# Optimization experiments

Measured on AMD Instinct MI355X. Metric: run time of the kernel, lower is better.

## Reference

```python
import jax, jax.numpy as jnp
import numpy as np

TEMP = 11.313708498984761  # sqrt(d_k=128)

def setup_inputs() -> dict:
    key = jax.random.key(0)
    ks = jax.random.split(key, 5)
    B, H, T, D = 8, 8, 1024, 128
    shp = (B, H, T, D)
    return {
        "q_time": jax.random.normal(ks[0], shp, dtype=jnp.float32),
        "k_time": jax.random.normal(ks[1], shp, dtype=jnp.float32),
        "q_feature": jax.random.normal(ks[2], shp, dtype=jnp.float32),
        "k_feature": jax.random.normal(ks[3], shp, dtype=jnp.float32),
        "v": jax.random.normal(ks[4], shp, dtype=jnp.float32),
    }

def reference(q_time, k_time, q_feature, k_feature, v):
    # time attention: [B,H,T,T]
    scores_t = jnp.einsum("bhtd,bhsd->bhts", q_time / TEMP, k_time)
    attn_time = jax.nn.softmax(scores_t, axis=-1)
    # feature attention: q_feature^T @ k_feature -> [B,H,D,D]
    scores_f = jnp.einsum("bhtd,bhte->bhde", q_feature / TEMP, k_feature)
    attn_feature = jax.nn.softmax(scores_f, axis=-1)
    # output = attn_time @ v @ attn_feature : [B,H,T,D]
    tv = jnp.einsum("bhts,bhsd->bhtd", attn_time, v)
    output = jnp.einsum("bhtd,bhde->bhte", tv, attn_feature)
    return output, attn_time, attn_feature
```

## Files before the change

kernel.cpp:

```cpp
#include <hip/hip_runtime.h>

typedef __bf16 bf16x8 __attribute__((ext_vector_type(8)));
typedef __bf16 bf16x4 __attribute__((ext_vector_type(4)));
typedef float f32x4 __attribute__((ext_vector_type(4)));

#define T_DIM 1024
#define D_DIM 128
#define NHEAD 64

static constexpr float INV_TEMP = 0.08838834764831845f;
static constexpr size_t OUT_ATTN = (size_t)NHEAD * T_DIM * D_DIM;
static constexpr size_t OUT_AF = OUT_ATTN + (size_t)NHEAD * T_DIM * T_DIM;

#define MFMA16 __builtin_amdgcn_mfma_f32_16x16x32_bf16

__device__ __forceinline__ int swz(int row, int col) {
  return (row << 7) + ((((col >> 3) ^ row) & 15) << 3) + (col & 7);
}

__device__ __forceinline__ bf16x8 ld8(const __bf16* buf, int row, int col) {
  return *reinterpret_cast<const bf16x8*>(&buf[swz(row, col)]);
}

__device__ __forceinline__ void nt_store4(float* dst, float a, float b, float c, float d) {
  f32x4 v = {a, b, c, d};
  __builtin_nontemporal_store(v, reinterpret_cast<f32x4*>(dst));
}

__device__ __forceinline__ void stage_f32_tile_128(const float* __restrict__ src,
                                                   __bf16* dst, int tid, float scale) {
  const float4* s4 = reinterpret_cast<const float4*>(src);
#pragma unroll
  for (int i = 0; i < 16; ++i) {
    int flat = i * 256 + tid;
    int row = flat >> 5;
    int c4 = (flat & 31) << 2;
    float4 vq = s4[flat];
    bf16x4 b;
    b[0] = (__bf16)(vq.x * scale);
    b[1] = (__bf16)(vq.y * scale);
    b[2] = (__bf16)(vq.z * scale);
    b[3] = (__bf16)(vq.w * scale);
    *reinterpret_cast<bf16x4*>(&dst[swz(row, c4)]) = b;
  }
}

__device__ __forceinline__ void stage_wt_tile(const __bf16* __restrict__ src,
                                              __bf16* dst, int tid) {
#pragma unroll
  for (int i = 0; i < 8; ++i) {
    int flat = i * 256 + tid;
    int row = flat >> 4;
    int c8 = (flat & 15) << 3;
    bf16x8 vv = *reinterpret_cast<const bf16x8*>(src + (size_t)row * T_DIM + c8);
    *reinterpret_cast<bf16x8*>(&dst[swz(row, c8)]) = vv;
  }
}

__device__ __forceinline__ void cp16_async(const void* g, void* l) {
  typedef __attribute__((address_space(1))) unsigned int gu32;
  typedef __attribute__((address_space(3))) unsigned int lu32;
  __builtin_amdgcn_global_load_lds((gu32*)g, (lu32*)l, 16, 0, 0);
}

__device__ __forceinline__ void stage_async_tile(const __bf16* __restrict__ gbase,
                                                 int row_stride_elems,
                                                 __bf16* lbuf, int tid) {
  const int w = tid >> 6;
  const int lane = tid & 63;
#pragma unroll
  for (int i = 0; i < 8; ++i) {
    int seg = i * 4 + w;
    int row = seg * 4 + (lane >> 4);
    int c = ((lane & 15) ^ row) & 15;
    const void* src = (const void*)(gbase + (size_t)row * row_stride_elems + c * 8);
    void* dst = (void*)(lbuf + seg * 512);
    cp16_async(src, dst);
  }
}

__device__ __forceinline__ void compute_S(const bf16x8 afrag[4][2], const __bf16* bufB,
                                          int l16, int quad, f32x4 sacc[2][8]) {
#pragma unroll
  for (int mt = 0; mt < 2; ++mt)
#pragma unroll
    for (int nt = 0; nt < 8; ++nt)
      sacc[mt][nt] = (f32x4){0.f, 0.f, 0.f, 0.f};
#pragma unroll
  for (int ki = 0; ki < 4; ++ki) {
    bf16x8 bfr[8];
#pragma unroll
    for (int nt = 0; nt < 8; ++nt)
      bfr[nt] = ld8(bufB, nt * 16 + l16, ki * 32 + quad * 8);
#pragma unroll
    for (int nt = 0; nt < 8; ++nt) {
      sacc[0][nt] = MFMA16(afrag[ki][0], bfr[nt], sacc[0][nt], 0, 0, 0);
      sacc[1][nt] = MFMA16(afrag[ki][1], bfr[nt], sacc[1][nt], 0, 0, 0);
    }
  }
}

__global__ __launch_bounds__(256, 2)
void cd_attn_feature(const float* __restrict__ qf, const float* __restrict__ kf,
                     float* __restrict__ out) {
  __shared__ __bf16 qfT[64][40];
  __shared__ __bf16 kfT[128][40];
  const int tid = threadIdx.x;
  const int w = tid >> 6;
  const int lane = tid & 63;
  const int quad = lane >> 4;
  const int l16 = lane & 15;
  const int head = blockIdx.x & 63;
  const int dstart = (blockIdx.x >> 6) << 6;

  const float* __restrict__ qfh = qf + (size_t)head * (T_DIM * D_DIM);
  const float* __restrict__ kfh = kf + (size_t)head * (T_DIM * D_DIM);

  f32x4 acc[8];
#pragma unroll
  for (int nt = 0; nt < 8; ++nt) acc[nt] = (f32x4){0.f, 0.f, 0.f, 0.f};

  for (int tc = 0; tc < T_DIM; tc += 32) {
    __syncthreads();
#pragma unroll
    for (int i = 0; i < 2; ++i) {
      int flat = i * 256 + tid;
      int t = flat >> 4;
      int d4 = (flat & 15) << 2;
      float4 vv = *reinterpret_cast<const float4*>(qfh + (size_t)(tc + t) * D_DIM + dstart + d4);
      qfT[d4 + 0][t] = (__bf16)vv.x;
      qfT[d4 + 1][t] = (__bf16)vv.y;
      qfT[d4 + 2][t] = (__bf16)vv.z;
      qfT[d4 + 3][t] = (__bf16)vv.w;
    }
#pragma unroll
    for (int i = 0; i < 4; ++i) {
      int flat = i * 256 + tid;
      int t = flat >> 5;
      int e4 = (flat & 31) << 2;
      float4 vv = *reinterpret_cast<const float4*>(kfh + (size_t)(tc + t) * D_DIM + e4);
      kfT[e4 + 0][t] = (__bf16)vv.x;
      kfT[e4 + 1][t] = (__bf16)vv.y;
      kfT[e4 + 2][t] = (__bf16)vv.z;
      kfT[e4 + 3][t] = (__bf16)vv.w;
    }
    __syncthreads();
    bf16x8 a = *reinterpret_cast<const bf16x8*>(&qfT[w * 16 + l16][quad * 8]);
#pragma unroll
    for (int nt = 0; nt < 8; ++nt) {
      bf16x8 b = *reinterpret_cast<const bf16x8*>(&kfT[nt * 16 + l16][quad * 8]);
      acc[nt] = MFMA16(a, b, acc[nt], 0, 0, 0);
    }
  }

  float p[8][4];
  float rsum[4] = {0.f, 0.f, 0.f, 0.f};
#pragma unroll
  for (int nt = 0; nt < 8; ++nt)
#pragma unroll
    for (int r = 0; r < 4; ++r) {
      p[nt][r] = __expf(acc[nt][r] * INV_TEMP);
      rsum[r] += p[nt][r];
    }
#pragma unroll
  for (int off = 1; off < 16; off <<= 1)
#pragma unroll
    for (int r = 0; r < 4; ++r)
      rsum[r] += __shfl_xor(rsum[r], off, 64);
#pragma unroll
  for (int r = 0; r < 4; ++r) rsum[r] = 1.0f / rsum[r];

  float* __restrict__ afh = out + OUT_AF + (size_t)head * (D_DIM * D_DIM);
#pragma unroll
  for (int nt = 0; nt < 8; ++nt)
#pragma unroll
    for (int r = 0; r < 4; ++r)
      afh[(size_t)(dstart + w * 16 + quad * 4 + r) * D_DIM + nt * 16 + l16] = p[nt][r] * rsum[r];
}

__global__ __launch_bounds__(256, 2)
void cd_attn_w(const float* __restrict__ v, const float* __restrict__ out_ro,
               __bf16* __restrict__ wt,
               const float* __restrict__ qt, const float* __restrict__ kt,
               __bf16* __restrict__ qtb, __bf16* __restrict__ ktb) {
  __shared__ __bf16 vt[128 * 128];
  __shared__ __bf16 aft[128 * 128];
  const int tid = threadIdx.x;
  const int w = tid >> 6;
  const int lane = tid & 63;
  const int quad = lane >> 4;
  const int l16 = lane & 15;
  const int head = blockIdx.x & 63;
  const int t0 = (blockIdx.x >> 6) << 7;

  if (qtb != nullptr) {
    const float4* q4 = reinterpret_cast<const float4*>(qt);
    const float4* k4 = reinterpret_cast<const float4*>(kt);
    size_t base = (size_t)blockIdx.x * 2048 + tid;
#pragma unroll
    for (int i = 0; i < 8; ++i) {
      size_t c = base + (size_t)(i * 256);
      float4 a = q4[c * 2], b = q4[c * 2 + 1];
      bf16x8 o;
      o[0] = (__bf16)(a.x * INV_TEMP); o[1] = (__bf16)(a.y * INV_TEMP);
      o[2] = (__bf16)(a.z * INV_TEMP); o[3] = (__bf16)(a.w * INV_TEMP);
      o[4] = (__bf16)(b.x * INV_TEMP); o[5] = (__bf16)(b.y * INV_TEMP);
      o[6] = (__bf16)(b.z * INV_TEMP); o[7] = (__bf16)(b.w * INV_TEMP);
      *reinterpret_cast<bf16x8*>(qtb + c * 8) = o;
      a = k4[c * 2]; b = k4[c * 2 + 1];
      o[0] = (__bf16)a.x; o[1] = (__bf16)a.y; o[2] = (__bf16)a.z; o[3] = (__bf16)a.w;
      o[4] = (__bf16)b.x; o[5] = (__bf16)b.y; o[6] = (__bf16)b.z; o[7] = (__bf16)b.w;
      *reinterpret_cast<bf16x8*>(ktb + c * 8) = o;
    }
  }

  const float* __restrict__ vh = v + (size_t)head * (T_DIM * D_DIM);
  const float* __restrict__ afh = out_ro + OUT_AF + (size_t)head * (D_DIM * D_DIM);

#pragma unroll
  for (int i = 0; i < 16; ++i) {
    int flat = i * 256 + tid;
    int d = flat >> 5;
    int e4 = (flat & 31) << 2;
    float4 vv = *reinterpret_cast<const float4*>(afh + (size_t)d * D_DIM + e4);
    aft[swz(e4 + 0, d)] = (__bf16)vv.x;
    aft[swz(e4 + 1, d)] = (__bf16)vv.y;
    aft[swz(e4 + 2, d)] = (__bf16)vv.z;
    aft[swz(e4 + 3, d)] = (__bf16)vv.w;
  }
  stage_f32_tile_128(vh + (size_t)t0 * D_DIM, vt, tid, 1.0f);
  __syncthreads();

  f32x4 acc[2][8];
#pragma unroll
  for (int mt = 0; mt < 2; ++mt)
#pragma unroll
    for (int nt = 0; nt < 8; ++nt) acc[mt][nt] = (f32x4){0.f, 0.f, 0.f, 0.f};

#pragma unroll
  for (int ki = 0; ki < 4; ++ki) {
    bf16x8 a0 = ld8(vt, w * 32 + l16, ki * 32 + quad * 8);
    bf16x8 a1 = ld8(vt, w * 32 + 16 + l16, ki * 32 + quad * 8);
#pragma unroll
    for (int nt = 0; nt < 8; ++nt) {
      bf16x8 b = ld8(aft, nt * 16 + l16, ki * 32 + quad * 8);
      acc[0][nt] = MFMA16(a0, b, acc[0][nt], 0, 0, 0);
      acc[1][nt] = MFMA16(a1, b, acc[1][nt], 0, 0, 0);
    }
  }

  __syncthreads();
#pragma unroll
  for (int mt = 0; mt < 2; ++mt)
#pragma unroll
    for (int nt = 0; nt < 8; ++nt)
#pragma unroll
      for (int r = 0; r < 4; ++r)
        aft[swz(nt * 16 + l16, w * 32 + mt * 16 + quad * 4 + r)] = (__bf16)acc[mt][nt][r];
  __syncthreads();

  __bf16* __restrict__ wth = wt + (size_t)head * (D_DIM * T_DIM);
#pragma unroll
  for (int i = 0; i < 8; ++i) {
    int row = i * 16 + (tid >> 4);
    int pc = tid & 15;
    bf16x8 vv = *reinterpret_cast<const bf16x8*>(&aft[(row << 7) + (pc << 3)]);
    int col = ((pc ^ row) & 15) << 3;
    *reinterpret_cast<bf16x8*>(&wth[(size_t)row * T_DIM + t0 + col]) = vv;
  }
}

__global__ __launch_bounds__(256, 2)
void cd_attn_time_v2(const __bf16* __restrict__ qtb, const __bf16* __restrict__ ktb,
                     const __bf16* __restrict__ wt, float* __restrict__ out) {
  __shared__ __align__(16) __bf16 lds_all[2 * 128 * 128];
  __bf16* buf0 = lds_all;
  __bf16* buf1 = lds_all + 128 * 128;
  const int tid = threadIdx.x;
  const int w = tid >> 6;
  const int lane = tid & 63;
  const int quad = lane >> 4;
  const int l16 = lane & 15;
  const int head = blockIdx.x & 63;
  const int t0 = (blockIdx.x >> 6) << 7;

  const __bf16* __restrict__ qth = qtb + (size_t)head * (T_DIM * D_DIM);
  const __bf16* __restrict__ kth = ktb + (size_t)head * (T_DIM * D_DIM);
  const __bf16* __restrict__ wth = wt + (size_t)head * (D_DIM * T_DIM);
  float* __restrict__ attn_out = out + OUT_ATTN + (size_t)head * ((size_t)T_DIM * T_DIM);
  float* __restrict__ o_out = out + (size_t)head * (T_DIM * D_DIM);

  stage_async_tile(kth, D_DIM, buf0, tid);
  bf16x8 afrag[4][2];
#pragma unroll
  for (int ki = 0; ki < 4; ++ki) {
#pragma unroll
    for (int mt = 0; mt < 2; ++mt)
      afrag[ki][mt] = *reinterpret_cast<const bf16x8*>(
          qth + (size_t)(t0 + w * 32 + mt * 16 + l16) * D_DIM + ki * 32 + quad * 8);
  }

  float rs[2][4] = {{0.f, 0.f, 0.f, 0.f}, {0.f, 0.f, 0.f, 0.f}};
  for (int j = 0; j < 8; ++j) {
    if (j < 7) {
      stage_async_tile(kth + (size_t)(j + 1) * (128 * D_DIM), D_DIM,
                       (j & 1) ? buf0 : buf1, tid);
      asm volatile("s_waitcnt vmcnt(8)" ::: "memory");
    } else {
      asm volatile("s_waitcnt vmcnt(0)" ::: "memory");
    }
    __builtin_amdgcn_s_barrier();
    f32x4 sacc[2][8];
    compute_S(afrag, (j & 1) ? buf1 : buf0, l16, quad, sacc);
#pragma unroll
    for (int mt = 0; mt < 2; ++mt)
#pragma unroll
      for (int nt = 0; nt < 8; ++nt)
#pragma unroll
        for (int r = 0; r < 4; ++r)
          rs[mt][r] += __expf(sacc[mt][nt][r]);
    asm volatile("s_waitcnt lgkmcnt(0)" ::: "memory");
    __builtin_amdgcn_s_barrier();
  }
#pragma unroll
  for (int off = 1; off < 16; off <<= 1)
#pragma unroll
    for (int mt = 0; mt < 2; ++mt)
#pragma unroll
      for (int r = 0; r < 4; ++r)
        rs[mt][r] += __shfl_xor(rs[mt][r], off, 64);
  float invl[2][4];
#pragma unroll
  for (int mt = 0; mt < 2; ++mt)
#pragma unroll
    for (int r = 0; r < 4; ++r)
      invl[mt][r] = 1.0f / rs[mt][r];

  f32x4 uacc[2][8];
#pragma unroll
  for (int mt = 0; mt < 2; ++mt)
#pragma unroll
    for (int nt = 0; nt < 8; ++nt) uacc[mt][nt] = (f32x4){0.f, 0.f, 0.f, 0.f};

  stage_async_tile(kth, D_DIM, buf0, tid);
  stage_async_tile(wth, T_DIM, buf1, tid);
  for (int j = 0; j < 8; ++j) {
    if (j == 0)
      asm volatile("s_waitcnt vmcnt(0)" ::: "memory");
    else
      asm volatile("s_waitcnt vmcnt(16)" ::: "memory");
    __builtin_amdgcn_s_barrier();
    f32x4 sacc[2][8];
    compute_S(afrag, buf0, l16, quad, sacc);
    asm volatile("s_waitcnt lgkmcnt(0)" ::: "memory");
    __builtin_amdgcn_s_barrier();
#pragma unroll
    for (int mt = 0; mt < 2; ++mt)
#pragma unroll
      for (int nt = 0; nt < 8; ++nt)
#pragma unroll
        for (int r = 0; r < 4; ++r)
          buf0[swz(w * 32 + mt * 16 + quad * 4 + r, nt * 16 + l16)] =
              (__bf16)(__expf(sacc[mt][nt][r]) * invl[mt][r]);
    asm volatile("s_waitcnt lgkmcnt(0)" ::: "memory");
#pragma unroll
    for (int ki = 0; ki < 4; ++ki) {
      bf16x8 aP0 = ld8(buf0, w * 32 + l16, ki * 32 + quad * 8);
      bf16x8 aP1 = ld8(buf0, w * 32 + 16 + l16, ki * 32 + quad * 8);
#pragma unroll
      for (int nt = 0; nt < 8; ++nt) {
        bf16x8 bW = ld8(buf1, nt * 16 + l16, ki * 32 + quad * 8);
        uacc[0][nt] = MFMA16(aP0, bW, uacc[0][nt], 0, 0, 0);
        uacc[1][nt] = MFMA16(aP1, bW, uacc[1][nt], 0, 0, 0);
      }
    }
    asm volatile("s_waitcnt lgkmcnt(0)" ::: "memory");
    __builtin_amdgcn_s_barrier();
    bf16x8 pv[8];
#pragma unroll
    for (int i = 0; i < 8; ++i) {
      int row = i * 16 + (tid >> 4);
      int pc = tid & 15;
      pv[i] = *reinterpret_cast<const bf16x8*>(&buf0[(row << 7) + (pc << 3)]);
    }
    asm volatile("s_waitcnt lgkmcnt(0)" ::: "memory");
    __builtin_amdgcn_s_barrier();
    if (j < 7) {
      stage_async_tile(kth + (size_t)(j + 1) * (128 * D_DIM), D_DIM, buf0, tid);
      stage_async_tile(wth + (size_t)(j + 1) * 128, T_DIM, buf1, tid);
    }
    asm volatile("" ::: "memory");
    __builtin_amdgcn_sched_barrier(0);
    const int s0 = j * 128;
#pragma unroll
    for (int i = 0; i < 8; ++i) {
      int row = i * 16 + (tid >> 4);
      int pc = tid & 15;
      int col = ((pc ^ row) & 15) << 3;
      float* dst = attn_out + (size_t)(t0 + row) * T_DIM + s0 + col;
      nt_store4(dst, (float)pv[i][0], (float)pv[i][1], (float)pv[i][2], (float)pv[i][3]);
      nt_store4(dst + 4, (float)pv[i][4], (float)pv[i][5], (float)pv[i][6], (float)pv[i][7]);
    }
  }

  float* fbuf = reinterpret_cast<float*>(lds_all);
#pragma unroll
  for (int mt = 0; mt < 2; ++mt)
#pragma unroll
    for (int nt = 0; nt < 8; ++nt)
#pragma unroll
      for (int r = 0; r < 4; ++r)
        fbuf[(w * 32 + mt * 16 + quad * 4 + r) * 128 + nt * 16 + l16] = uacc[mt][nt][r];
  asm volatile("s_waitcnt lgkmcnt(0)" ::: "memory");
  __builtin_amdgcn_s_barrier();
#pragma unroll
  for (int i = 0; i < 16; ++i) {
    int flat = i * 256 + tid;
    int row = flat >> 5;
    int c4 = (flat & 31) << 2;
    f32x4 vv = *reinterpret_cast<const f32x4*>(&fbuf[row * 128 + c4]);
    __builtin_nontemporal_store(
        vv, reinterpret_cast<f32x4*>(o_out + (size_t)(t0 + row) * D_DIM + c4));
  }
}

__global__ __launch_bounds__(256, 2)
void cd_attn_time(const float* __restrict__ qt, const float* __restrict__ kt,
                  const __bf16* __restrict__ wt, float* __restrict__ out) {
  __shared__ __bf16 bufB[128 * 128];
  __shared__ __bf16 bufP[128 * 128];
  const int tid = threadIdx.x;
  const int w = tid >> 6;
  const int lane = tid & 63;
  const int quad = lane >> 4;
  const int l16 = lane & 15;
  const int head = blockIdx.x & 63;
  const int t0 = (blockIdx.x >> 6) << 7;

  const float* __restrict__ qth = qt + (size_t)head * (T_DIM * D_DIM);
  const float* __restrict__ kth = kt + (size_t)head * (T_DIM * D_DIM);
  const __bf16* __restrict__ wth = wt + (size_t)head * (D_DIM * T_DIM);
  float* __restrict__ attn_out = out + OUT_ATTN + (size_t)head * ((size_t)T_DIM * T_DIM);
  float* __restrict__ o_out = out + (size_t)head * (T_DIM * D_DIM);

  stage_f32_tile_128(qth + (size_t)t0 * D_DIM, bufB, tid, INV_TEMP);
  __syncthreads();
  bf16x8 afrag[4][2];
#pragma unroll
  for (int ki = 0; ki < 4; ++ki) {
    afrag[ki][0] = ld8(bufB, w * 32 + l16, ki * 32 + quad * 8);
    afrag[ki][1] = ld8(bufB, w * 32 + 16 + l16, ki * 32 + quad * 8);
  }

  float rs[2][4] = {{0.f, 0.f, 0.f, 0.f}, {0.f, 0.f, 0.f, 0.f}};
  for (int j = 0; j < 8; ++j) {
    __syncthreads();
    stage_f32_tile_128(kth + (size_t)(j * 128) * D_DIM, bufB, tid, 1.0f);
    __syncthreads();
    f32x4 sacc[2][8];
    compute_S(afrag, bufB, l16, quad, sacc);
#pragma unroll
    for (int mt = 0; mt < 2; ++mt)
#pragma unroll
      for (int nt = 0; nt < 8; ++nt)
#pragma unroll
        for (int r = 0; r < 4; ++r)
          rs[mt][r] += __expf(sacc[mt][nt][r]);
  }
#pragma unroll
  for (int off = 1; off < 16; off <<= 1)
#pragma unroll
    for (int mt = 0; mt < 2; ++mt)
#pragma unroll
      for (int r = 0; r < 4; ++r)
        rs[mt][r] += __shfl_xor(rs[mt][r], off, 64);
  float invl[2][4];
#pragma unroll
  for (int mt = 0; mt < 2; ++mt)
#pragma unroll
    for (int r = 0; r < 4; ++r)
      invl[mt][r] = 1.0f / rs[mt][r];

  f32x4 uacc[2][8];
#pragma unroll
  for (int mt = 0; mt < 2; ++mt)
#pragma unroll
    for (int nt = 0; nt < 8; ++nt) uacc[mt][nt] = (f32x4){0.f, 0.f, 0.f, 0.f};

  for (int j = 0; j < 8; ++j) {
    __syncthreads();
    stage_f32_tile_128(kth + (size_t)(j * 128) * D_DIM, bufB, tid, 1.0f);
    __syncthreads();
    f32x4 sacc[2][8];
    compute_S(afrag, bufB, l16, quad, sacc);
    __syncthreads();
    stage_wt_tile(wth + j * 128, bufB, tid);
#pragma unroll
    for (int mt = 0; mt < 2; ++mt)
#pragma unroll
      for (int nt = 0; nt < 8; ++nt)
#pragma unroll
        for (int r = 0; r < 4; ++r) {
          float p = __expf(sacc[mt][nt][r]) * invl[mt][r];
          bufP[swz(w * 32 + mt * 16 + quad * 4 + r, nt * 16 + l16)] = (__bf16)p;
        }
    __syncthreads();
    const int s0 = j * 128;
#pragma unroll
    for (int i = 0; i < 8; ++i) {
      int row = i * 16 + (tid >> 4);
      int pc = tid & 15;
      bf16x8 pv = *reinterpret_cast<const bf16x8*>(&bufP[(row << 7) + (pc << 3)]);
      int col = ((pc ^ row) & 15) << 3;
      float4 o1, o2;
      o1.x = (float)pv[0]; o1.y = (float)pv[1]; o1.z = (float)pv[2]; o1.w = (float)pv[3];
      o2.x = (float)pv[4]; o2.y = (float)pv[5]; o2.z = (float)pv[6]; o2.w = (float)pv[7];
      float4* dstp = reinterpret_cast<float4*>(attn_out + (size_t)(t0 + row) * T_DIM + s0 + col);
      dstp[0] = o1;
      dstp[1] = o2;
    }
#pragma unroll
    for (int ki = 0; ki < 4; ++ki) {
      bf16x8 aP0 = ld8(bufP, w * 32 + l16, ki * 32 + quad * 8);
      bf16x8 aP1 = ld8(bufP, w * 32 + 16 + l16, ki * 32 + quad * 8);
#pragma unroll
      for (int nt = 0; nt < 8; ++nt) {
        bf16x8 bW = ld8(bufB, nt * 16 + l16, ki * 32 + quad * 8);
        uacc[0][nt] = MFMA16(aP0, bW, uacc[0][nt], 0, 0, 0);
        uacc[1][nt] = MFMA16(aP1, bW, uacc[1][nt], 0, 0, 0);
      }
    }
  }

#pragma unroll
  for (int mt = 0; mt < 2; ++mt)
#pragma unroll
    for (int nt = 0; nt < 8; ++nt)
#pragma unroll
      for (int r = 0; r < 4; ++r)
        o_out[(size_t)(t0 + w * 32 + mt * 16 + quad * 4 + r) * D_DIM + nt * 16 + l16] =
            uacc[mt][nt][r];
}

extern "C" void kernel_launch(void* const* d_in, const int* in_sizes, int n_in,
                              void* d_out, int out_size, void* d_ws, size_t ws_size,
                              hipStream_t stream) {
  (void)in_sizes; (void)n_in; (void)out_size;
  const float* q_time    = (const float*)d_in[0];
  const float* k_time    = (const float*)d_in[1];
  const float* q_feature = (const float*)d_in[2];
  const float* k_feature = (const float*)d_in[3];
  const float* v         = (const float*)d_in[4];
  float* out = (float*)d_out;
  __bf16* wt = (__bf16*)d_ws;

  const size_t NELEM = (size_t)NHEAD * T_DIM * D_DIM;
  const size_t WS_NEED = NELEM * 2 * 3;

  if (ws_size >= WS_NEED) {
    __bf16* qtb = wt + NELEM;
    __bf16* ktb = qtb + NELEM;
    cd_attn_feature<<<128, 256, 0, stream>>>(q_feature, k_feature, out);
    cd_attn_w<<<512, 256, 0, stream>>>(v, out, wt, q_time, k_time, qtb, ktb);
    cd_attn_time_v2<<<512, 256, 0, stream>>>(qtb, ktb, wt, out);
  } else {
    cd_attn_w<<<512, 256, 0, stream>>>(v, out, wt, nullptr, nullptr, nullptr, nullptr);
    cd_attn_time<<<512, 256, 0, stream>>>(q_time, k_time, wt, out);
  }
}
```

Measured before the change: 680.0 us.

## Double query rows per block to share K and W tiles across eight waves

The time-attention kernel now uses 512-thread blocks covering 256 query rows, so each staged K and W tile in LDS serves twice as many rows and fewer blocks reload the same data. The first pass moves from a double buffer to a triple buffer for K, prefetching two tiles ahead and issuing the next load after the barrier. P is written into a split slab (S2 for the first four waves, S0 for the rest), and the output epilogue is done in two halves. LDS use rises to 96KB per block, and only 256 blocks are launched, which may lower occupancy and latency hiding. The fallback path also gains a feature-attention launch.

Result: slower. 712.6 us (+4.8%).

```diff
diff --git a/kernel.cpp b/kernel.cpp
--- a/kernel.cpp
+++ b/kernel.cpp
@@ -63,14 +63,14 @@
   __builtin_amdgcn_global_load_lds((gu32*)g, (lu32*)l, 16, 0, 0);
 }
 
-__device__ __forceinline__ void stage_async_tile(const __bf16* __restrict__ gbase,
-                                                 int row_stride_elems,
-                                                 __bf16* lbuf, int tid) {
+__device__ __forceinline__ void stage_async_tile512(const __bf16* __restrict__ gbase,
+                                                    int row_stride_elems,
+                                                    __bf16* lbuf, int tid) {
   const int w = tid >> 6;
   const int lane = tid & 63;
 #pragma unroll
-  for (int i = 0; i < 8; ++i) {
-    int seg = i * 4 + w;
+  for (int i = 0; i < 4; ++i) {
+    int seg = i * 8 + w;
     int row = seg * 4 + (lane >> 4);
     int c = ((lane & 15) ^ row) & 15;
     const void* src = (const void*)(gbase + (size_t)row * row_stride_elems + c * 8);
@@ -270,19 +270,20 @@
   }
 }
 
-__global__ __launch_bounds__(256, 2)
-void cd_attn_time_v2(const __bf16* __restrict__ qtb, const __bf16* __restrict__ ktb,
+__global__ __launch_bounds__(512, 2)
+void cd_attn_time_v3(const __bf16* __restrict__ qtb, const __bf16* __restrict__ ktb,
                      const __bf16* __restrict__ wt, float* __restrict__ out) {
-  __shared__ __align__(16) __bf16 lds_all[2 * 128 * 128];
-  __bf16* buf0 = lds_all;
-  __bf16* buf1 = lds_all + 128 * 128;
+  __shared__ __align__(16) __bf16 lds_all[3 * 16384];
+  __bf16* S0 = lds_all;
+  __bf16* S1 = lds_all + 16384;
+  __bf16* S2 = lds_all + 32768;
   const int tid = threadIdx.x;
   const int w = tid >> 6;
   const int lane = tid & 63;
   const int quad = lane >> 4;
   const int l16 = lane & 15;
   const int head = blockIdx.x & 63;
-  const int t0 = (blockIdx.x >> 6) << 7;
+  const int t0 = (blockIdx.x >> 6) << 8;
 
   const __bf16* __restrict__ qth = qtb + (size_t)head * (T_DIM * D_DIM);
   const __bf16* __restrict__ kth = ktb + (size_t)head * (T_DIM * D_DIM);
@@ -290,7 +291,8 @@
   float* __restrict__ attn_out = out + OUT_ATTN + (size_t)head * ((size_t)T_DIM * T_DIM);
   float* __restrict__ o_out = out + (size_t)head * (T_DIM * D_DIM);
 
-  stage_async_tile(kth, D_DIM, buf0, tid);
+  stage_async_tile512(kth, D_DIM, S0, tid);
+  stage_async_tile512(kth + (size_t)128 * D_DIM, D_DIM, S1, tid);
   bf16x8 afrag[4][2];
 #pragma unroll
   for (int ki = 0; ki < 4; ++ki) {
@@ -302,16 +304,16 @@
 
   float rs[2][4] = {{0.f, 0.f, 0.f, 0.f}, {0.f, 0.f, 0.f, 0.f}};
   for (int j = 0; j < 8; ++j) {
-    if (j < 7) {
-      stage_async_tile(kth + (size_t)(j + 1) * (128 * D_DIM), D_DIM,
-                       (j & 1) ? buf0 : buf1, tid);
-      asm volatile("s_waitcnt vmcnt(8)" ::: "memory");
-    } else {
+    if (j < 7)
+      asm volatile("s_waitcnt vmcnt(4)" ::: "memory");
+    else
       asm volatile("s_waitcnt vmcnt(0)" ::: "memory");
-    }
-    __builtin_amdgcn_s_barrier();
+    __builtin_amdgcn_s_barrier();
+    if (j < 6)
+      stage_async_tile512(kth + (size_t)(j + 2) * (128 * D_DIM), D_DIM,
+                          lds_all + ((j + 2) % 3) * 16384, tid);
     f32x4 sacc[2][8];
-    compute_S(afrag, (j & 1) ? buf1 : buf0, l16, quad, sacc);
+    compute_S(afrag, lds_all + (j % 3) * 16384, l16, quad, sacc);
 #pragma unroll
     for (int mt = 0; mt < 2; ++mt)
 #pragma unroll
@@ -342,8 +344,11 @@
 #pragma unroll
     for (int nt = 0; nt < 8; ++nt) uacc[mt][nt] = (f32x4){0.f, 0.f, 0.f, 0.f};
 
-  stage_async_tile(kth, D_DIM, buf0, tid);
-  stage_async_tile(wth, T_DIM, buf1, tid);
+  __bf16* pslab = (w < 4) ? S2 : S0;
+  const int prow0 = (w & 3) * 32;
+
+  stage_async_tile512(kth, D_DIM, S0, tid);
+  stage_async_tile512(wth, T_DIM, S1, tid);
   for (int j = 0; j < 8; ++j) {
     if (j == 0)
       asm volatile("s_waitcnt vmcnt(0)" ::: "memory");
@@ -351,7 +356,7 @@
       asm volatile("s_waitcnt vmcnt(16)" ::: "memory");
     __builtin_amdgcn_s_barrier();
     f32x4 sacc[2][8];
-    compute_S(afrag, buf0, l16, quad, sacc);
+    compute_S(afrag, S0, l16, quad, sacc);
     asm volatile("s_waitcnt lgkmcnt(0)" ::: "memory");
     __builtin_amdgcn_s_barrier();
 #pragma unroll
@@ -360,16 +365,16 @@
       for (int nt = 0; nt < 8; ++nt)
 #pragma unroll
         for (int r = 0; r < 4; ++r)
-          buf0[swz(w * 32 + mt * 16 + quad * 4 + r, nt * 16 + l16)] =
+          pslab[swz(prow0 + mt * 16 + quad * 4 + r, nt * 16 + l16)] =
               (__bf16)(__expf(sacc[mt][nt][r]) * invl[mt][r]);
     asm volatile("s_waitcnt lgkmcnt(0)" ::: "memory");
 #pragma unroll
     for (int ki = 0; ki < 4; ++ki) {
-      bf16x8 aP0 = ld8(buf0, w * 32 + l16, ki * 32 + quad * 8);
-      bf16x8 aP1 = ld8(buf0, w * 32 + 16 + l16, ki * 32 + quad * 8);
+      bf16x8 aP0 = ld8(pslab, prow0 + l16, ki * 32 + quad * 8);
+      bf16x8 aP1 = ld8(pslab, prow0 + 16 + l16, ki * 32 + quad * 8);
 #pragma unroll
       for (int nt = 0; nt < 8; ++nt) {
-        bf16x8 bW = ld8(buf1, nt * 16 + l16, ki * 32 + quad * 8);
+        bf16x8 bW = ld8(S1, nt * 16 + l16, ki * 32 + quad * 8);
         uacc[0][nt] = MFMA16(aP0, bW, uacc[0][nt], 0, 0, 0);
         uacc[1][nt] = MFMA16(aP1, bW, uacc[1][nt], 0, 0, 0);
       }
@@ -377,25 +382,25 @@
     asm volatile("s_waitcnt lgkmcnt(0)" ::: "memory");
     __builtin_amdgcn_s_barrier();
     bf16x8 pv[8];
+    const int pc = tid & 15;
 #pragma unroll
     for (int i = 0; i < 8; ++i) {
-      int row = i * 16 + (tid >> 4);
-      int pc = tid & 15;
-      pv[i] = *reinterpret_cast<const bf16x8*>(&buf0[(row << 7) + (pc << 3)]);
+      int row = i * 32 + (tid >> 4);
+      const __bf16* pb = (row < 128) ? S2 : S0;
+      pv[i] = *reinterpret_cast<const bf16x8*>(&pb[((row & 127) << 7) + (pc << 3)]);
     }
     asm volatile("s_waitcnt lgkmcnt(0)" ::: "memory");
     __builtin_amdgcn_s_barrier();
     if (j < 7) {
-      stage_async_tile(kth + (size_t)(j + 1) * (128 * D_DIM), D_DIM, buf0, tid);
-      stage_async_tile(wth + (size_t)(j + 1) * 128, T_DIM, buf1, tid);
+      stage_async_tile512(kth + (size_t)(j + 1) * (128 * D_DIM), D_DIM, S0, tid);
+      stage_async_tile512(wth + (size_t)(j + 1) * 128, T_DIM, S1, tid);
     }
     asm volatile("" ::: "memory");
     __builtin_amdgcn_sched_barrier(0);
     const int s0 = j * 128;
 #pragma unroll
     for (int i = 0; i < 8; ++i) {
-      int row = i * 16 + (tid >> 4);
-      int pc = tid & 15;
+      int row = i * 32 + (tid >> 4);
       int col = ((pc ^ row) & 15) << 3;
       float* dst = attn_out + (size_t)(t0 + row) * T_DIM + s0 + col;
       nt_store4(dst, (float)pv[i][0], (float)pv[i][1], (float)pv[i][2], (float)pv[i][3]);
@@ -405,22 +410,30 @@
 
   float* fbuf = reinterpret_cast<float*>(lds_all);
 #pragma unroll
-  for (int mt = 0; mt < 2; ++mt)
-#pragma unroll
-    for (int nt = 0; nt < 8; ++nt)
-#pragma unroll
-      for (int r = 0; r < 4; ++r)
-        fbuf[(w * 32 + mt * 16 + quad * 4 + r) * 128 + nt * 16 + l16] = uacc[mt][nt][r];
-  asm volatile("s_waitcnt lgkmcnt(0)" ::: "memory");
-  __builtin_amdgcn_s_barrier();
-#pragma unroll
-  for (int i = 0; i < 16; ++i) {
-    int flat = i * 256 + tid;
-    int row = flat >> 5;
-    int c4 = (flat & 31) << 2;
-    f32x4 vv = *reinterpret_cast<const f32x4*>(&fbuf[row * 128 + c4]);
-    __builtin_nontemporal_store(
-        vv, reinterpret_cast<f32x4*>(o_out + (size_t)(t0 + row) * D_DIM + c4));
+  for (int h = 0; h < 2; ++h) {
+    if ((w >> 2) == h) {
+#pragma unroll
+      for (int mt = 0; mt < 2; ++mt)
+#pragma unroll
+        for (int nt = 0; nt < 8; ++nt)
+#pragma unroll
+          for (int r = 0; r < 4; ++r)
+            fbuf[((w & 3) * 32 + mt * 16 + quad * 4 + r) * 128 + nt * 16 + l16] =
+                uacc[mt][nt][r];
+    }
+    asm volatile("s_waitcnt lgkmcnt(0)" ::: "memory");
+    __builtin_amdgcn_s_barrier();
+#pragma unroll
+    for (int i = 0; i < 8; ++i) {
+      int flat = i * 512 + tid;
+      int row = flat >> 5;
+      int c4 = (flat & 31) << 2;
+      f32x4 vv = *reinterpret_cast<const f32x4*>(&fbuf[row * 128 + c4]);
+      __builtin_nontemporal_store(
+          vv, reinterpret_cast<f32x4*>(o_out + (size_t)(t0 + h * 128 + row) * D_DIM + c4));
+    }
+    asm volatile("s_waitcnt lgkmcnt(0)" ::: "memory");
+    __builtin_amdgcn_s_barrier();
   }
 }
 
@@ -562,8 +575,9 @@
     __bf16* ktb = qtb + NELEM;
     cd_attn_feature<<<128, 256, 0, stream>>>(q_feature, k_feature, out);
     cd_attn_w<<<512, 256, 0, stream>>>(v, out, wt, q_time, k_time, qtb, ktb);
-    cd_attn_time_v2<<<512, 256, 0, stream>>>(qtb, ktb, wt, out);
+    cd_attn_time_v3<<<256, 512, 0, stream>>>(qtb, ktb, wt, out);
   } else {
+    cd_attn_feature<<<128, 256, 0, stream>>>(q_feature, k_feature, out);
     cd_attn_w<<<512, 256, 0, stream>>>(v, out, wt, nullptr, nullptr, nullptr, nullptr);
     cd_attn_time<<<512, 256, 0, stream>>>(q_time, k_time, wt, out);
   }
```

## Move q/k time bf16 conversion into feature kernel and prefetch feature tiles

Applied to the files above, without the earlier changes.

The q_time/k_time fp32-to-bf16 conversion moves out of cd_attn_w into 256 extra blocks of cd_attn_feature, which before had only 128 blocks and left most CUs idle. Those conversion blocks run alongside the feature-attention GEMM blocks. The feature GEMM loop now loads the next T-chunk of qf/kf into registers before the barrier (register double buffering), so global-load latency overlaps the MFMA work. The fallback path now also launches cd_attn_feature, which fixes a missing attn_feature computation on that path.

Result: faster. 617.3 us (-9.2%).

```diff
diff --git a/kernel.cpp b/kernel.cpp
--- a/kernel.cpp
+++ b/kernel.cpp
@@ -102,103 +102,18 @@
 
 __global__ __launch_bounds__(256, 2)
 void cd_attn_feature(const float* __restrict__ qf, const float* __restrict__ kf,
-                     float* __restrict__ out) {
-  __shared__ __bf16 qfT[64][40];
-  __shared__ __bf16 kfT[128][40];
+                     float* __restrict__ out,
+                     const float* __restrict__ qt, const float* __restrict__ kt,
+                     __bf16* __restrict__ qtb, __bf16* __restrict__ ktb) {
   const int tid = threadIdx.x;
-  const int w = tid >> 6;
-  const int lane = tid & 63;
-  const int quad = lane >> 4;
-  const int l16 = lane & 15;
-  const int head = blockIdx.x & 63;
-  const int dstart = (blockIdx.x >> 6) << 6;
-
-  const float* __restrict__ qfh = qf + (size_t)head * (T_DIM * D_DIM);
-  const float* __restrict__ kfh = kf + (size_t)head * (T_DIM * D_DIM);
-
-  f32x4 acc[8];
-#pragma unroll
-  for (int nt = 0; nt < 8; ++nt) acc[nt] = (f32x4){0.f, 0.f, 0.f, 0.f};
-
-  for (int tc = 0; tc < T_DIM; tc += 32) {
-    __syncthreads();
-#pragma unroll
-    for (int i = 0; i < 2; ++i) {
-      int flat = i * 256 + tid;
-      int t = flat >> 4;
-      int d4 = (flat & 15) << 2;
-      float4 vv = *reinterpret_cast<const float4*>(qfh + (size_t)(tc + t) * D_DIM + dstart + d4);
-      qfT[d4 + 0][t] = (__bf16)vv.x;
-      qfT[d4 + 1][t] = (__bf16)vv.y;
-      qfT[d4 + 2][t] = (__bf16)vv.z;
-      qfT[d4 + 3][t] = (__bf16)vv.w;
-    }
-#pragma unroll
-    for (int i = 0; i < 4; ++i) {
-      int flat = i * 256 + tid;
-      int t = flat >> 5;
-      int e4 = (flat & 31) << 2;
-      float4 vv = *reinterpret_cast<const float4*>(kfh + (size_t)(tc + t) * D_DIM + e4);
-      kfT[e4 + 0][t] = (__bf16)vv.x;
-      kfT[e4 + 1][t] = (__bf16)vv.y;
-      kfT[e4 + 2][t] = (__bf16)vv.z;
-      kfT[e4 + 3][t] = (__bf16)vv.w;
-    }
-    __syncthreads();
-    bf16x8 a = *reinterpret_cast<const bf16x8*>(&qfT[w * 16 + l16][quad * 8]);
-#pragma unroll
-    for (int nt = 0; nt < 8; ++nt) {
-      bf16x8 b = *reinterpret_cast<const bf16x8*>(&kfT[nt * 16 + l16][quad * 8]);
-      acc[nt] = MFMA16(a, b, acc[nt], 0, 0, 0);
-    }
-  }
-
-  float p[8][4];
-  float rsum[4] = {0.f, 0.f, 0.f, 0.f};
-#pragma unroll
-  for (int nt = 0; nt < 8; ++nt)
-#pragma unroll
-    for (int r = 0; r < 4; ++r) {
-      p[nt][r] = __expf(acc[nt][r] * INV_TEMP);
-      rsum[r] += p[nt][r];
-    }
-#pragma unroll
-  for (int off = 1; off < 16; off <<= 1)
-#pragma unroll
-    for (int r = 0; r < 4; ++r)
-      rsum[r] += __shfl_xor(rsum[r], off, 64);
-#pragma unroll
-  for (int r = 0; r < 4; ++r) rsum[r] = 1.0f / rsum[r];
-
-  float* __restrict__ afh = out + OUT_AF + (size_t)head * (D_DIM * D_DIM);
-#pragma unroll
-  for (int nt = 0; nt < 8; ++nt)
-#pragma unroll
-    for (int r = 0; r < 4; ++r)
-      afh[(size_t)(dstart + w * 16 + quad * 4 + r) * D_DIM + nt * 16 + l16] = p[nt][r] * rsum[r];
-}
-
-__global__ __launch_bounds__(256, 2)
-void cd_attn_w(const float* __restrict__ v, const float* __restrict__ out_ro,
-               __bf16* __restrict__ wt,
-               const float* __restrict__ qt, const float* __restrict__ kt,
-               __bf16* __restrict__ qtb, __bf16* __restrict__ ktb) {
-  __shared__ __bf16 vt[128 * 128];
-  __shared__ __bf16 aft[128 * 128];
-  const int tid = threadIdx.x;
-  const int w = tid >> 6;
-  const int lane = tid & 63;
-  const int quad = lane >> 4;
-  const int l16 = lane & 15;
-  const int head = blockIdx.x & 63;
-  const int t0 = (blockIdx.x >> 6) << 7;
-
-  if (qtb != nullptr) {
+
+  if (blockIdx.x >= 128) {
+    const int pbid = blockIdx.x - 128;
     const float4* q4 = reinterpret_cast<const float4*>(qt);
     const float4* k4 = reinterpret_cast<const float4*>(kt);
-    size_t base = (size_t)blockIdx.x * 2048 + tid;
-#pragma unroll
-    for (int i = 0; i < 8; ++i) {
+    size_t base = (size_t)pbid * 4096 + tid;
+#pragma unroll
+    for (int i = 0; i < 16; ++i) {
       size_t c = base + (size_t)(i * 256);
       float4 a = q4[c * 2], b = q4[c * 2 + 1];
       bf16x8 o;
@@ -212,7 +127,112 @@
       o[4] = (__bf16)b.x; o[5] = (__bf16)b.y; o[6] = (__bf16)b.z; o[7] = (__bf16)b.w;
       *reinterpret_cast<bf16x8*>(ktb + c * 8) = o;
     }
-  }
+    return;
+  }
+
+  __shared__ __bf16 qfT[64][40];
+  __shared__ __bf16 kfT[128][40];
+  const int w = tid >> 6;
+  const int lane = tid & 63;
+  const int quad = lane >> 4;
+  const int l16 = lane & 15;
+  const int head = blockIdx.x & 63;
+  const int dstart = (blockIdx.x >> 6) << 6;
+
+  const float* __restrict__ qfh = qf + (size_t)head * (T_DIM * D_DIM);
+  const float* __restrict__ kfh = kf + (size_t)head * (T_DIM * D_DIM);
+
+  f32x4 acc[8];
+#pragma unroll
+  for (int nt = 0; nt < 8; ++nt) acc[nt] = (f32x4){0.f, 0.f, 0.f, 0.f};
+
+  const int qt_ = tid >> 4, qd4 = (tid & 15) << 2;
+  const int kt_ = tid >> 5, ke4 = (tid & 31) << 2;
+
+  float4 qreg[2], kreg[4];
+#pragma unroll
+  for (int i = 0; i < 2; ++i)
+    qreg[i] = *reinterpret_cast<const float4*>(
+        qfh + (size_t)(i * 16 + qt_) * D_DIM + dstart + qd4);
+#pragma unroll
+  for (int i = 0; i < 4; ++i)
+    kreg[i] = *reinterpret_cast<const float4*>(
+        kfh + (size_t)(i * 8 + kt_) * D_DIM + ke4);
+
+  for (int tc = 0; tc < T_DIM; tc += 32) {
+    __syncthreads();
+#pragma unroll
+    for (int i = 0; i < 2; ++i) {
+      int t = i * 16 + qt_;
+      qfT[qd4 + 0][t] = (__bf16)qreg[i].x;
+      qfT[qd4 + 1][t] = (__bf16)qreg[i].y;
+      qfT[qd4 + 2][t] = (__bf16)qreg[i].z;
+      qfT[qd4 + 3][t] = (__bf16)qreg[i].w;
+    }
+#pragma unroll
+    for (int i = 0; i < 4; ++i) {
+      int t = i * 8 + kt_;
+      kfT[ke4 + 0][t] = (__bf16)kreg[i].x;
+      kfT[ke4 + 1][t] = (__bf16)kreg[i].y;
+      kfT[ke4 + 2][t] = (__bf16)kreg[i].z;
+      kfT[ke4 + 3][t] = (__bf16)kreg[i].w;
+    }
+    if (tc + 32 < T_DIM) {
+#pragma unroll
+      for (int i = 0; i < 2; ++i)
+        qreg[i] = *reinterpret_cast<const float4*>(
+            qfh + (size_t)(tc + 32 + i * 16 + qt_) * D_DIM + dstart + qd4);
+#pragma unroll
+      for (int i = 0; i < 4; ++i)
+        kreg[i] = *reinterpret_cast<const float4*>(
+            kfh + (size_t)(tc + 32 + i * 8 + kt_) * D_DIM + ke4);
+    }
+    __syncthreads();
+    bf16x8 a = *reinterpret_cast<const bf16x8*>(&qfT[w * 16 + l16][quad * 8]);
+#pragma unroll
+    for (int nt = 0; nt < 8; ++nt) {
+      bf16x8 b = *reinterpret_cast<const bf16x8*>(&kfT[nt * 16 + l16][quad * 8]);
+      acc[nt] = MFMA16(a, b, acc[nt], 0, 0, 0);
+    }
+  }
+
+  float p[8][4];
+  float rsum[4] = {0.f, 0.f, 0.f, 0.f};
+#pragma unroll
+  for (int nt = 0; nt < 8; ++nt)
+#pragma unroll
+    for (int r = 0; r < 4; ++r) {
+      p[nt][r] = __expf(acc[nt][r] * INV_TEMP);
+      rsum[r] += p[nt][r];
+    }
+#pragma unroll
+  for (int off = 1; off < 16; off <<= 1)
+#pragma unroll
+    for (int r = 0; r < 4; ++r)
+      rsum[r] += __shfl_xor(rsum[r], off, 64);
+#pragma unroll
+  for (int r = 0; r < 4; ++r) rsum[r] = 1.0f / rsum[r];
+
+  float* __restrict__ afh = out + OUT_AF + (size_t)head * (D_DIM * D_DIM);
+#pragma unroll
+  for (int nt = 0; nt < 8; ++nt)
+#pragma unroll
+    for (int r = 0; r < 4; ++r)
+      afh[(size_t)(dstart + w * 16 + quad * 4 + r) * D_DIM + nt * 16 + l16] = p[nt][r] * rsum[r];
+}
+
+__global__ __launch_bounds__(256, 2)
+void cd_attn_w(const float* __restrict__ v, const float* __restrict__ out_ro,
+               __bf16* __restrict__ wt) {
+  __shared__ __bf16 vt[128 * 128];
+  __shared__ __bf16 aft[128 * 128];
+  const int tid = threadIdx.x;
+  const int w = tid >> 6;
+  const int lane = tid & 63;
+  const int quad = lane >> 4;
+  const int l16 = lane & 15;
+  const int head = blockIdx.x & 63;
+  const int t0 = (blockIdx.x >> 6) << 7;
 
   const float* __restrict__ vh = v + (size_t)head * (T_DIM * D_DIM);
   const float* __restrict__ afh = out_ro + OUT_AF + (size_t)head * (D_DIM * D_DIM);
@@ -560,11 +580,14 @@
   if (ws_size >= WS_NEED) {
     __bf16* qtb = wt + NELEM;
     __bf16* ktb = qtb + NELEM;
-    cd_attn_feature<<<128, 256, 0, stream>>>(q_feature, k_feature, out);
-    cd_attn_w<<<512, 256, 0, stream>>>(v, out, wt, q_time, k_time, qtb, ktb);
+    cd_attn_feature<<<384, 256, 0, stream>>>(q_feature, k_feature, out,
+                                             q_time, k_time, qtb, ktb);
+    cd_attn_w<<<512, 256, 0, stream>>>(v, out, wt);
     cd_attn_time_v2<<<512, 256, 0, stream>>>(qtb, ktb, wt, out);
   } else {
-    cd_attn_w<<<512, 256, 0, stream>>>(v, out, wt, nullptr, nullptr, nullptr, nullptr);
+    cd_attn_feature<<<128, 256, 0, stream>>>(q_feature, k_feature, out,
+                                             nullptr, nullptr, nullptr, nullptr);
+    cd_attn_w<<<512, 256, 0, stream>>>(v, out, wt);
     cd_attn_time<<<512, 256, 0, stream>>>(q_time, k_time, wt, out);
   }
 }
```
